# Kernel tuning notes

Measured on AMD Instinct MI355X. Metric: run time of the kernel, lower is better.

The kernel has to match this reference:

```python
import jax, jax.numpy as jnp
import numpy as np

B, S, T, E, H, Vt, Vs, M = 16, 64, 64, 256, 512, 32000, 32000, 100
J = 2 * M + 1


def _lstm(x, lengths, Wx, Wh, b, reverse=False):
    # TF LSTMCell (forget_bias=1.0) with sequence_length masking, optional reverse_sequence.
    Bn, Tn, _ = x.shape
    Hn = Wh.shape[0]
    tpos = jnp.arange(Tn)
    ridx = None
    if reverse:
        ridx = jnp.where(tpos[None, :] < lengths[:, None], lengths[:, None] - 1 - tpos[None, :], tpos[None, :])
        x = jnp.take_along_axis(x, ridx[:, :, None], axis=1)
    mask = (tpos[:, None] < lengths[None, :])[:, :, None]  # [T,B,1]
    xT = jnp.swapaxes(x, 0, 1)  # [T,B,E]

    def step(carry, inp):
        h, c = carry
        xt, mt = inp
        g = xt @ Wx + h @ Wh + b
        i, j, f, o = jnp.split(g, 4, axis=-1)
        c_new = jax.nn.sigmoid(f + 1.0) * c + jax.nn.sigmoid(i) * jnp.tanh(j)
        h_new = jax.nn.sigmoid(o) * jnp.tanh(c_new)
        c2 = jnp.where(mt, c_new, c)
        h2 = jnp.where(mt, h_new, h)
        return (h2, c2), jnp.where(mt, h_new, jnp.zeros_like(h_new))

    init = (jnp.zeros((Bn, Hn), x.dtype), jnp.zeros((Bn, Hn), x.dtype))
    _, ys = jax.lax.scan(step, init, (xT, mask))
    ys = jnp.swapaxes(ys, 0, 1)  # [B,T,H]
    if reverse:
        ys = jnp.take_along_axis(ys, ridx[:, :, None], axis=1)
    return ys


def setup_inputs() -> dict:
    key = jax.random.key(0)
    ks = jax.random.split(key, 24)
    sc = 0.05
    n = lambda k, shape: (jax.random.normal(k, shape, jnp.float32) * sc)
    inp = {
        "sources": jax.random.randint(ks[0], (B, S), 0, Vs, jnp.int32),
        "targets": jax.random.randint(ks[1], (B, T), 0, Vt, jnp.int32),
        "targets_null": jnp.array([Vt - 1], jnp.int32),
        "target_lengths": jax.random.randint(ks[2], (B,), T // 2, T + 1, jnp.int32),
        "emb": n(ks[3], (Vt, E)),
        "nnW": n(ks[4], (E, H)),
        "nnb": jnp.zeros((H,), jnp.float32),
        "Wx_fw": n(ks[5], (E, 4 * H)),
        "Wh_fw": n(ks[6], (H, 4 * H)),
        "b_fw": jnp.zeros((4 * H,), jnp.float32),
        "Wx_bw": n(ks[7], (E, 4 * H)),
        "Wh_bw": n(ks[8], (H, 4 * H)),
        "b_bw": jnp.zeros((4 * H,), jnp.float32),
        "Wproj_e": n(ks[9], (2 * H, H)),
        "Wv": n(ks[10], (H, Vs)),
        "bv": jnp.zeros((Vs,), jnp.float32),
        "Wproj_t": n(ks[11], (2 * H, E)),
        "Wj": n(ks[12], (H, J)),
        "bj": jnp.zeros((J,), jnp.float32),
        "Wp0": n(ks[13], (H, 1)),
        "bp0": jnp.zeros((1,), jnp.float32),
    }
    return inp


def reference(sources, targets, targets_null, target_lengths, emb, nnW, nnb,
              Wx_fw, Wh_fw, b_fw, Wx_bw, Wh_bw, b_bw, Wproj_e, Wv, bv,
              Wproj_t, Wj, bj, Wp0, bp0):
    x = emb[targets]                              # [B,T,E]
    x_null = emb[targets_null]                    # [1,E]
    null_state = jnp.tanh(x_null @ nnW + nnb)     # [1,H]
    h_fw = _lstm(x, target_lengths, Wx_fw, Wh_fw, b_fw, False)
    h_bw = _lstm(x, target_lengths, Wx_bw, Wh_bw, b_bw, True)
    h_cat = jnp.concatenate([h_fw, h_bw], axis=-1)  # [B,T,2H]

    # ---- emission ----
    ts = h_cat @ Wproj_e                          # [B,T,H]
    probs = jax.nn.softmax(ts @ Wv + bv, axis=-1)             # [B,T,Vs]
    null_probs = jax.nn.softmax(null_state @ Wv + bv, axis=-1)  # [1,Vs]
    e_word = jnp.take_along_axis(probs, sources[:, None, :].astype(jnp.int32), axis=2)  # [B,T,S]
    e_null = jnp.broadcast_to(null_probs[0][sources][:, None, :], e_word.shape)
    emission = jnp.concatenate([e_word, e_null], axis=1)       # [B,2T,S]

    # ---- transition ----
    tt = jnp.tanh((h_cat @ Wproj_t) @ nnW + nnb)  # [B,T,H]
    jump = jax.nn.softmax(tt @ Wj + bj, axis=-1)  # [B,T,J]
    p0 = jax.nn.sigmoid(tt @ Wp0 + bp0)[..., 0]   # [B,T]
    Tn = targets.shape[1]
    # entry (i,j) <- jump[i, M + j - i] (the tf.map_fn gather over word_idx)
    idx = M + jnp.arange(Tn)[None, :] - jnp.arange(Tn)[:, None]  # [T,T]
    jw = jnp.take_along_axis(jump, jnp.broadcast_to(idx[None], (jump.shape[0], Tn, Tn)), axis=2)  # [B,T,T]
    eye = jnp.eye(Tn, dtype=jw.dtype)
    half = jnp.concatenate([jw, p0[:, :, None] * eye], axis=2)            # [B,T,2T]
    transition = jnp.concatenate([half, half], axis=1)                    # [B,2T,2T]
    lhalf = jnp.concatenate([jnp.log(jw), jnp.log(p0)[:, :, None] * eye], axis=2)
    transition_log = jnp.concatenate([lhalf, lhalf], axis=1)
    return emission, transition, transition_log
```

## Files before the change

kernel.cpp:

```cpp
#include <hip/hip_runtime.h>
#include <hip/hip_bf16.h>
#include <math.h>

#define Bn 16
#define Sn 64
#define Tn 64
#define En 256
#define Hn 512
#define VS 32000
#define Jn 201
#define Mn 100

#define O_HCATF  0
#define O_DENOM  524288
#define O_NULLD  525312
#define O_SLOTS  525376
#define O_HBUF   527424
#define ZERO_N   560192
#define O_NS     560192
#define O_TS     560704
#define O_TSF    1084992
#define O_TTPRE  1347136
#define O_TTPF   1609280
#define O_TT     1740352
#define O_XF     2264640
#define O_WVC    2264640
#define O_WXFW   2395712
#define O_WXBW   2657856
#define O_WPEF   2920000
#define O_WPTF   3182144
#define O_NNWF   3313216
#define O_GX     3378752

typedef __attribute__((ext_vector_type(8))) short short8;
typedef __attribute__((ext_vector_type(4))) float f32x4;

__device__ __forceinline__ float sigf(float x) { return 1.0f / (1.0f + expf(-x)); }
__device__ __forceinline__ unsigned short tobf(float x) {
    __hip_bfloat16 h = __float2bfloat16(x);
    return *reinterpret_cast<unsigned short*>(&h);
}

__device__ __forceinline__ void dconvA(const float* __restrict__ A, uint4* __restrict__ out,
                                       int K, const int* __restrict__ gidx, int g) {
    int Kd = K >> 5;
    int lane = g & 63, t = g >> 6;
    int ks = t % Kd, mt = t / Kd;
    int m = mt * 16 + (lane & 15);
    int k0 = ks * 32 + (lane >> 4) * 8;
    const float* p = (gidx ? A + (size_t)gidx[m] * K : A + (size_t)m * K) + k0;
    float4 f0 = *(const float4*)(p);
    float4 f1 = *(const float4*)(p + 4);
    unsigned short u[8] = {tobf(f0.x), tobf(f0.y), tobf(f0.z), tobf(f0.w),
                           tobf(f1.x), tobf(f1.y), tobf(f1.z), tobf(f1.w)};
    out[g] = *(uint4*)u;
}

__device__ __forceinline__ void dconvB(const float* __restrict__ B, uint4* __restrict__ out,
                                       int N, int K, int g) {
    int Kd = K >> 5;
    int lane = g & 63, t = g >> 6;
    int ks = t % Kd, nt = t / Kd;
    int n = nt * 16 + (lane & 15);
    int k0 = ks * 32 + (lane >> 4) * 8;
    const float* p = B + (size_t)k0 * N + n;
    unsigned short u[8];
#pragma unroll
    for (int j = 0; j < 8; j++) u[j] = tobf(p[(size_t)j * N]);
    out[g] = *(uint4*)u;
}

__global__ __launch_bounds__(256) void convA2_k(const float* __restrict__ ttpre,
                                                uint4* __restrict__ ttpf,
                                                const float* __restrict__ ts,
                                                uint4* __restrict__ tsf) {
    int blk = blockIdx.x, tid = threadIdx.x;
    if (blk < 128) dconvA(ttpre, ttpf, 256, nullptr, blk * 256 + tid);
    else           dconvA(ts, tsf, 512, nullptr, (blk - 128) * 256 + tid);
}

__global__ __launch_bounds__(256) void mega_prep_k(float4* __restrict__ zdst, int zn4,
                                                   const float* __restrict__ emb,
                                                   const int* __restrict__ targets,
                                                   uint4* __restrict__ xf,
                                                   const float* __restrict__ wxfw, uint4* __restrict__ wxfwf,
                                                   const float* __restrict__ wxbw, uint4* __restrict__ wxbwf) {
    int blk = blockIdx.x, tid = threadIdx.x;
    if (blk < 548) {
        int i = blk * 256 + tid;
        if (i < zn4) zdst[i] = make_float4(0.f, 0.f, 0.f, 0.f);
    } else if (blk < 676) {
        dconvA(emb, xf, 256, targets, (blk - 548) * 256 + tid);
    } else if (blk < 932) {
        dconvB(wxfw, wxfwf, 2048, 256, (blk - 676) * 256 + tid);
    } else {
        dconvB(wxbw, wxbwf, 2048, 256, (blk - 932) * 256 + tid);
    }
}

template <int ACT>
__device__ __forceinline__ void gemm_body(const uint4* __restrict__ af,
                                          const uint4* __restrict__ bf,
                                          const float* __restrict__ bias,
                                          float* __restrict__ C, int N, int Kd,
                                          int bx, int by) {
    int tid = threadIdx.x, w = tid >> 6, lane = tid & 63;
    int ntb = bx * 8 + w * 2;
    int mtb = by * 8;
    f32x4 acc[8][2];
#pragma unroll
    for (int i = 0; i < 8; i++)
#pragma unroll
        for (int j = 0; j < 2; j++) acc[i][j] = 0.0f;
    for (int ks = 0; ks < Kd; ++ks) {
        uint4 b0 = bf[(size_t)(ntb * Kd + ks) * 64 + lane];
        uint4 b1 = bf[(size_t)((ntb + 1) * Kd + ks) * 64 + lane];
#pragma unroll
        for (int i = 0; i < 8; i++) {
            uint4 a = af[(size_t)((mtb + i) * Kd + ks) * 64 + lane];
            acc[i][0] = __builtin_amdgcn_mfma_f32_16x16x32_bf16(
                *reinterpret_cast<short8*>(&a), *reinterpret_cast<short8*>(&b0), acc[i][0], 0, 0, 0);
            acc[i][1] = __builtin_amdgcn_mfma_f32_16x16x32_bf16(
                *reinterpret_cast<short8*>(&a), *reinterpret_cast<short8*>(&b1), acc[i][1], 0, 0, 0);
        }
    }
    int n0 = ntb * 16 + (lane & 15);
    int q = lane >> 4;
    float bs0 = bias ? bias[n0] : 0.f;
    float bs1 = bias ? bias[n0 + 16] : 0.f;
#pragma unroll
    for (int i = 0; i < 8; i++)
#pragma unroll
        for (int r = 0; r < 4; r++) {
            int m = (mtb + i) * 16 + q * 4 + r;
            float v0 = acc[i][0][r] + bs0;
            float v1 = acc[i][1][r] + bs1;
            if (ACT == 1) { v0 = tanhf(v0); v1 = tanhf(v1); }
            C[(size_t)m * N + n0] = v0;
            C[(size_t)m * N + n0 + 16] = v1;
        }
}

template <int ACT>
__global__ __launch_bounds__(256) void gemm_mfma_k(const uint4* __restrict__ af,
                                                   const uint4* __restrict__ bf,
                                                   const float* __restrict__ bias,
                                                   float* __restrict__ C, int N, int Kd) {
    gemm_body<ACT>(af, bf, bias, C, N, Kd, blockIdx.x, blockIdx.y);
}

__global__ __launch_bounds__(256) void gx_gemm_k(const uint4* __restrict__ xf,
                                                 const uint4* __restrict__ wxfwf,
                                                 const uint4* __restrict__ wxbwf,
                                                 const float* __restrict__ b_fw,
                                                 const float* __restrict__ b_bw,
                                                 float* __restrict__ gx) {
    int bx = blockIdx.x;
    if (bx < 16) gemm_body<0>(xf, wxfwf, b_fw, gx, 2048, 8, bx, blockIdx.y);
    else         gemm_body<0>(xf, wxbwf, b_bw, gx + 2097152, 2048, 8, bx - 16, blockIdx.y);
}

__global__ __launch_bounds__(256) void proj_gemm_k(const uint4* __restrict__ hcatf,
                                                   const uint4* __restrict__ wpef,
                                                   const uint4* __restrict__ wptf,
                                                   float* __restrict__ ts,
                                                   float* __restrict__ ttpre) {
    int bx = blockIdx.x;
    if (bx < 4) gemm_body<0>(hcatf, wpef, nullptr, ts, 512, 32, bx, blockIdx.y);
    else        gemm_body<0>(hcatf, wptf, nullptr, ttpre, 256, 32, bx - 4, blockIdx.y);
}

__global__ __launch_bounds__(256, 1) void lstm_fused_k(const float* __restrict__ wh_fw,
                                                       const float* __restrict__ wh_bw,
                                                       const float* __restrict__ gx,
                                                       const int* __restrict__ lengths,
                                                       unsigned* __restrict__ hbuf32,
                                                       unsigned* __restrict__ hcat32,
                                                       unsigned* __restrict__ slots,
                                                       const float* __restrict__ Wv,
                                                       const float* __restrict__ emb,
                                                       const int* __restrict__ tnull,
                                                       const float* __restrict__ nnW,
                                                       const float* __restrict__ nnb,
                                                       const float* __restrict__ bv,
                                                       float* __restrict__ ns,
                                                       float* __restrict__ nd,
                                                       const int* __restrict__ sources,
                                                       float* __restrict__ wvc,
                                                       const float* __restrict__ wpe, uint4* __restrict__ wpef,
                                                       const float* __restrict__ wpt, uint4* __restrict__ wptf,
                                                       const float* __restrict__ nnw2, uint4* __restrict__ nnwf) {
    int blk = blockIdx.x;
    int tid = threadIdx.x;

    if (blk >= 669) {
        dconvB(nnw2, nnwf, 512, 256, (blk - 669) * 256 + tid);
        return;
    }
    if (blk >= 541) {
        dconvB(wpt, wptf, 256, 1024, (blk - 541) * 256 + tid);
        return;
    }
    if (blk >= 285) {
        dconvB(wpe, wpef, 512, 1024, (blk - 285) * 256 + tid);
        return;
    }
    if (blk >= 157) {
        int cb = blk - 157;
#pragma unroll
        for (int cc = 0; cc < 8; ++cc) {
            int ci = cb * 8 + cc;
            int c = sources[ci];
            float v0 = Wv[(size_t)tid * VS + c];
            float v1 = Wv[(size_t)(tid + 256) * VS + c];
            wvc[(size_t)ci * 512 + tid] = v0;
            wvc[(size_t)ci * 512 + 256 + tid] = v1;
        }
        return;
    }
    if (blk >= 32) {
        __shared__ float xn[En];
        __shared__ float nsl[Hn];
        __shared__ float red[4];
        int bid = blk - 32;
        xn[tid] = emb[(size_t)tnull[0] * En + tid];
        __syncthreads();
#pragma unroll
        for (int hh = 0; hh < 2; hh++) {
            int h = tid + hh * 256;
            float a = nnb[h];
            for (int e = 0; e < En; e++) a += xn[e] * nnW[(size_t)e * Hn + h];
            float v = tanhf(a);
            nsl[h] = v;
            if (bid == 0) ns[h] = v;
        }
        __syncthreads();
        int v = bid * 256 + tid;
        float a = bv[v];
        for (int k = 0; k < Hn; k++) a += nsl[k] * Wv[(size_t)k * VS + v];
        float e = expf(a);
        for (int o = 1; o < 64; o <<= 1) e += __shfl_xor(e, o);
        if ((tid & 63) == 0) red[tid >> 6] = e;
        __syncthreads();
        if (tid == 0) atomicAdd(nd, red[0] + red[1] + red[2] + red[3]);
        return;
    }

    __shared__ uint4 whf[8192];
    __shared__ float raw[32][129];
    __shared__ int lenS[16];
    int dir = blk >> 4;
    int u0 = (blk & 15) * 32;
    const float* wh = dir ? wh_bw : wh_fw;
    if (tid < 16) lenS[tid] = lengths[tid];

    for (int chunk = 0; chunk < 16; ++chunk) {
#pragma unroll
        for (int it = 0; it < 16; ++it) {
            int li = it * 256 + tid;
            int kl = li >> 7, c = li & 127;
            int g = c >> 5, ub = c & 31;
            raw[kl][c] = wh[(size_t)(chunk * 32 + kl) * 2048 + g * 512 + u0 + ub];
        }
        __syncthreads();
#pragma unroll
        for (int it = 0; it < 2; ++it) {
            int idx = tid * 2 + it;
            int w = idx >> 7, t = (idx >> 6) & 1, lane = idx & 63;
            int n = lane & 15, uu = n >> 1, p = n & 1;
            int cc = (t * 2 + p) * 32 + w * 8 + uu;
            int kb = (lane >> 4) * 8;
            unsigned short u8[8];
#pragma unroll
            for (int j = 0; j < 8; j++) u8[j] = tobf(raw[kb + j][cc]);
            whf[((w * 2 + t) * 16 + chunk) * 64 + lane] = *(uint4*)u8;
        }
        __syncthreads();
    }

    int wv = tid >> 6, lane = tid & 63;
    int n = lane & 15, uu = n >> 1, q = lane >> 4;
    int u = u0 + wv * 8 + uu;
    float creg[4] = {0.f, 0.f, 0.f, 0.f};
    unsigned short hbf[4] = {0, 0, 0, 0};

    for (int s = 0; s < 64; ++s) {
        float gxi[4], gxj[4], gxf[4], gxo[4];
#pragma unroll
        for (int r = 0; r < 4; r++) {
            int b = q * 4 + r;
            int len = lenS[b];
            int tc = dir ? (len - 1 - s) : s;
            tc = tc < 0 ? 0 : tc;
            const float* gp = gx + (size_t)dir * 2097152 + (size_t)(b * 64 + tc) * 2048 + u;
            gxi[r] = gp[0]; gxj[r] = gp[512]; gxf[r] = gp[1024]; gxo[r] = gp[1536];
        }
        const unsigned long long* hb64 =
            (const unsigned long long*)(hbuf32 + (((s & 1) * 2 + dir) * 16) * 256);
        unsigned long long h64[32];
#pragma unroll
        for (int ks = 0; ks < 16; ks++) {
            int idx = n * 128 + ks * 8 + q * 2;
            h64[2 * ks] = __hip_atomic_load(hb64 + idx, __ATOMIC_RELAXED, __HIP_MEMORY_SCOPE_AGENT);
            h64[2 * ks + 1] = __hip_atomic_load(hb64 + idx + 1, __ATOMIC_RELAXED, __HIP_MEMORY_SCOPE_AGENT);
        }
        f32x4 acc0 = {0.f, 0.f, 0.f, 0.f}, acc1 = {0.f, 0.f, 0.f, 0.f};
#pragma unroll
        for (int ks = 0; ks < 16; ks++) {
            unsigned long long av[2] = {h64[2 * ks], h64[2 * ks + 1]};
            short8 a = *reinterpret_cast<short8*>(av);
            uint4 b0 = whf[((wv * 2 + 0) * 16 + ks) * 64 + lane];
            uint4 b1 = whf[((wv * 2 + 1) * 16 + ks) * 64 + lane];
            acc0 = __builtin_amdgcn_mfma_f32_16x16x32_bf16(a, *reinterpret_cast<short8*>(&b0), acc0, 0, 0, 0);
            acc1 = __builtin_amdgcn_mfma_f32_16x16x32_bf16(a, *reinterpret_cast<short8*>(&b1), acc1, 0, 0, 0);
        }
#pragma unroll
        for (int r = 0; r < 4; r++) {
            float jvv = __shfl_xor(acc0[r], 1);
            float ovv = __shfl_xor(acc1[r], 1);
            int b = q * 4 + r;
            int len = lenS[b];
            float gi = acc0[r] + gxi[r];
            float gj = jvv + gxj[r];
            float gf = acc1[r] + gxf[r];
            float go = ovv + gxo[r];
            float cn = sigf(gf + 1.0f) * creg[r] + sigf(gi) * tanhf(gj);
            float hn = sigf(go) * tanhf(cn);
            if (s < len) { creg[r] = cn; hbf[r] = tobf(hn); }
        }
#pragma unroll
        for (int r = 0; r < 4; r++) {
            unsigned self = hbf[r];
            unsigned part = (unsigned)__shfl_xor((int)self, 2) & 0xffffu;
            if ((n & 3) == 0) {
                unsigned pk = self | (part << 16);
                int b = q * 4 + r;
                __hip_atomic_store(
                    hbuf32 + ((((s + 1) & 1) * 2 + dir) * 16 + b) * 256 + (u >> 1), pk,
                    __ATOMIC_RELAXED, __HIP_MEMORY_SCOPE_AGENT);
                int len = lenS[b];
                if (s < len) {
                    int tin = dir ? (len - 1 - s) : s;
                    int row = b * 64 + tin, col = dir * 512 + u;
                    int mt = row >> 4, ksx = col >> 5;
                    int lanep = (row & 15) | (((col >> 3) & 3) << 4);
                    hcat32[(size_t)(((mt * 32 + ksx) * 64 + lanep) * 4) + ((col & 7) >> 1)] = pk;
                }
            }
        }
        if (s == 63) break;
        __syncthreads();
        if (tid == 0)
            __hip_atomic_store(&slots[blk * 64], (unsigned)(s + 1), __ATOMIC_RELAXED,
                               __HIP_MEMORY_SCOPE_AGENT);
        if (tid < 16) {
            while (__hip_atomic_load(&slots[(dir * 16 + tid) * 64], __ATOMIC_RELAXED,
                                     __HIP_MEMORY_SCOPE_AGENT) < (unsigned)(s + 1)) {
                __builtin_amdgcn_s_sleep(1);
            }
        }
        __syncthreads();
    }
}

__global__ __launch_bounds__(256) void phaseA_mfma_k(const uint4* __restrict__ tsb,
                                                     const float* __restrict__ Wv,
                                                     const float* __restrict__ bv,
                                                     float* __restrict__ denom) {
    __shared__ uint4 wls[8192];
    __shared__ float redL[4][128];
    int tid = threadIdx.x;
    int wave = tid >> 6, lane = tid & 63;
    for (int it = 0; it < 32; ++it) {
        int g = it * 256 + tid;
        int gl = g & 63, t = g >> 6;
        int ks = t & 15, tl = t >> 4;
        int nt = blockIdx.x * 8 + tl;
        int nn = nt * 16 + (gl & 15);
        int k0 = ks * 32 + (gl >> 4) * 8;
        const float* p = Wv + (size_t)k0 * VS + nn;
        unsigned short u[8];
#pragma unroll
        for (int j = 0; j < 8; j++) u[j] = tobf(p[(size_t)j * VS]);
        wls[g] = *(uint4*)u;
    }
    __syncthreads();

    int ntbase = blockIdx.x * 8 + wave * 2;
    float bv0 = bv[ntbase * 16 + (lane & 15)];
    float bv1 = bv[(ntbase + 1) * 16 + (lane & 15)];
    int q = lane >> 4;
    for (int mc = 0; mc < 8; ++mc) {
        f32x4 acc[8][2];
#pragma unroll
        for (int i = 0; i < 8; i++)
#pragma unroll
            for (int j = 0; j < 2; j++) acc[i][j] = 0.0f;
#pragma unroll 4
        for (int ks = 0; ks < 16; ++ks) {
            short8 a[8], b[2];
#pragma unroll
            for (int i = 0; i < 8; i++) {
                int mt = mc * 8 + i;
                uint4 t = tsb[(size_t)(mt * 16 + ks) * 64 + lane];
                a[i] = *reinterpret_cast<short8*>(&t);
            }
#pragma unroll
            for (int j = 0; j < 2; j++) {
                uint4 t = wls[((wave * 2 + j) * 16 + ks) * 64 + lane];
                b[j] = *reinterpret_cast<short8*>(&t);
            }
#pragma unroll
            for (int i = 0; i < 8; i++)
#pragma unroll
                for (int j = 0; j < 2; j++)
                    acc[i][j] = __builtin_amdgcn_mfma_f32_16x16x32_bf16(a[i], b[j], acc[i][j], 0, 0, 0);
        }
#pragma unroll
        for (int i = 0; i < 8; i++) {
#pragma unroll
            for (int r = 0; r < 4; r++) {
                float e = __expf(acc[i][0][r] + bv0) + __expf(acc[i][1][r] + bv1);
                e += __shfl_xor(e, 1);
                e += __shfl_xor(e, 2);
                e += __shfl_xor(e, 4);
                e += __shfl_xor(e, 8);
                if ((lane & 15) == 0) redL[wave][i * 16 + q * 4 + r] = e;
            }
        }
        __syncthreads();
        if (tid < 128) {
            float v = redL[0][tid] + redL[1][tid] + redL[2][tid] + redL[3][tid];
            atomicAdd(&denom[mc * 128 + tid], v);
        }
        __syncthreads();
    }
}

__global__ __launch_bounds__(512) void emission_k(const float* __restrict__ ts,
                                                  const float* __restrict__ wvc,
                                                  const float* __restrict__ bv,
                                                  const int* __restrict__ sources,
                                                  const float* __restrict__ ns,
                                                  const float* __restrict__ denom,
                                                  const float* __restrict__ nulld,
                                                  float* __restrict__ em) {
    __shared__ float colv[512];
    __shared__ float red[64][9];
    __shared__ float red2[8];
    __shared__ float env_s, bvc_s;
    int b = blockIdx.y, sc = blockIdx.x;
    int tid = threadIdx.x;
    for (int qq = 0; qq < 8; ++qq) {
        int s = sc * 8 + qq;
        int ci = b * 64 + s;
        __syncthreads();
        colv[tid] = wvc[(size_t)ci * 512 + tid];
        if (tid == 0) bvc_s = bv[sources[ci]];
        __syncthreads();
        int r = tid & 63, ksl = tid >> 6;
        const float* tr = ts + (size_t)(b * 64 + r) * 512 + ksl * 64;
        float p = 0.f;
#pragma unroll
        for (int k4 = 0; k4 < 16; k4++) {
            float4 t4 = *(const float4*)(tr + k4 * 4);
            float4 c4 = *(const float4*)&colv[ksl * 64 + k4 * 4];
            p += t4.x * c4.x + t4.y * c4.y + t4.z * c4.z + t4.w * c4.w;
        }
        red[r][ksl] = p;
        if (tid < 8) {
            float pn = 0.f;
#pragma unroll
            for (int k4 = 0; k4 < 16; k4++) {
                float4 n4 = *(const float4*)(ns + tid * 64 + k4 * 4);
                float4 c4 = *(const float4*)&colv[tid * 64 + k4 * 4];
                pn += n4.x * c4.x + n4.y * c4.y + n4.z * c4.z + n4.w * c4.w;
            }
            red2[tid] = pn;
        }
        __syncthreads();
        if (tid < 64) {
            float dot = red[tid][0] + red[tid][1] + red[tid][2] + red[tid][3] +
                        red[tid][4] + red[tid][5] + red[tid][6] + red[tid][7];
            float ew = expf(dot + bvc_s) / denom[b * 64 + tid];
            em[(size_t)(b * 128 + tid) * 64 + s] = ew;
        } else if (tid == 64) {
            float dn = red2[0] + red2[1] + red2[2] + red2[3] +
                       red2[4] + red2[5] + red2[6] + red2[7];
            env_s = expf(dn + bvc_s) / nulld[0];
        }
        __syncthreads();
        if (tid < 64) em[(size_t)(b * 128 + 64 + tid) * 64 + s] = env_s;
    }
}

__global__ __launch_bounds__(256) void transition_k(const float* __restrict__ tt,
                                                    const float* __restrict__ Wj,
                                                    const float* __restrict__ bj,
                                                    const float* __restrict__ Wp0,
                                                    const float* __restrict__ bp0,
                                                    float* __restrict__ trans,
                                                    float* __restrict__ tlog) {
    __shared__ float ttl[512];
    __shared__ float jrow[Jn], ljrow[Jn];
    __shared__ float sred[256];
    __shared__ float p0_s, lp0_s;
    int blk = blockIdx.x;
    int b = blk >> 6, i = blk & 63;
    int tid = threadIdx.x;
    {
        const float* trr = tt + (size_t)blk * 512;
        if (tid < 128) *(float4*)&ttl[tid * 4] = *(const float4*)(trr + tid * 4);
    }
    __syncthreads();
    bool isj = tid < Jn;
    bool isp = tid == Jn;
    float l = 0.f;
    if (isj || isp) {
        const float* wb = isj ? (Wj + tid) : Wp0;
        int stride = isj ? Jn : 1;
        float a = isj ? bj[tid] : bp0[0];
        for (int k = 0; k < 512; k++) a += ttl[k] * wb[(size_t)k * stride];
        l = a;
    }
    sred[tid] = isj ? l : -1e30f;
    __syncthreads();
    for (int o = 128; o > 0; o >>= 1) {
        if (tid < o) sred[tid] = fmaxf(sred[tid], sred[tid + o]);
        __syncthreads();
    }
    float m = sred[0];
    __syncthreads();
    float ex = isj ? expf(l - m) : 0.f;
    sred[tid] = ex;
    __syncthreads();
    for (int o = 128; o > 0; o >>= 1) {
        if (tid < o) sred[tid] += sred[tid + o];
        __syncthreads();
    }
    float S = sred[0];
    if (isj) {
        jrow[tid] = ex / S;
        ljrow[tid] = (l - m) - logf(S);
    }
    if (isp) {
        float pv = 1.f / (1.f + expf(-l));
        p0_s = pv;
        lp0_s = logf(pv);
    }
    __syncthreads();
    if (tid < 128) {
        int j = tid;
        float tv, lv;
        if (j < 64) {
            int id = Mn + j - i;
            tv = jrow[id];
            lv = ljrow[id];
        } else {
            bool dg = (j - 64) == i;
            tv = dg ? p0_s : 0.f;
            lv = dg ? lp0_s : 0.f;
        }
        size_t r1 = (size_t)(b * 128 + i) * 128 + j;
        size_t r2 = (size_t)(b * 128 + 64 + i) * 128 + j;
        trans[r1] = tv;
        trans[r2] = tv;
        tlog[r1] = lv;
        tlog[r2] = lv;
    }
}

extern "C" void kernel_launch(void* const* d_in, const int* in_sizes, int n_in,
                              void* d_out, int out_size, void* d_ws, size_t ws_size,
                              hipStream_t stream) {
    const int* sources = (const int*)d_in[0];
    const int* targets = (const int*)d_in[1];
    const int* tnull = (const int*)d_in[2];
    const int* lengths = (const int*)d_in[3];
    const float* emb = (const float*)d_in[4];
    const float* nnW = (const float*)d_in[5];
    const float* nnb = (const float*)d_in[6];
    const float* Wx_fw = (const float*)d_in[7];
    const float* Wh_fw = (const float*)d_in[8];
    const float* b_fw = (const float*)d_in[9];
    const float* Wx_bw = (const float*)d_in[10];
    const float* Wh_bw = (const float*)d_in[11];
    const float* b_bw = (const float*)d_in[12];
    const float* Wproj_e = (const float*)d_in[13];
    const float* Wv = (const float*)d_in[14];
    const float* bv = (const float*)d_in[15];
    const float* Wproj_t = (const float*)d_in[16];
    const float* Wj = (const float*)d_in[17];
    const float* bj = (const float*)d_in[18];
    const float* Wp0 = (const float*)d_in[19];
    const float* bp0 = (const float*)d_in[20];

    float* ws = (float*)d_ws;
    float* out = (float*)d_out;
    float* out_em = out;
    float* out_tr = out + 131072;
    float* out_tl = out + 131072 + 262144;

    mega_prep_k<<<1188, 256, 0, stream>>>((float4*)ws, ZERO_N / 4,
                                          emb, targets, (uint4*)(ws + O_XF),
                                          Wx_fw, (uint4*)(ws + O_WXFW),
                                          Wx_bw, (uint4*)(ws + O_WXBW));

    gx_gemm_k<<<dim3(32, 8), 256, 0, stream>>>((uint4*)(ws + O_XF), (uint4*)(ws + O_WXFW),
                                               (uint4*)(ws + O_WXBW), b_fw, b_bw, ws + O_GX);

    lstm_fused_k<<<733, 256, 0, stream>>>(Wh_fw, Wh_bw, ws + O_GX, lengths,
                                          (unsigned*)(ws + O_HBUF), (unsigned*)(ws + O_HCATF),
                                          (unsigned*)(ws + O_SLOTS),
                                          Wv, emb, tnull, nnW, nnb, bv,
                                          ws + O_NS, ws + O_NULLD,
                                          sources, ws + O_WVC,
                                          Wproj_e, (uint4*)(ws + O_WPEF),
                                          Wproj_t, (uint4*)(ws + O_WPTF),
                                          nnW, (uint4*)(ws + O_NNWF));

    proj_gemm_k<<<dim3(6, 8), 256, 0, stream>>>((uint4*)(ws + O_HCATF), (uint4*)(ws + O_WPEF),
                                                (uint4*)(ws + O_WPTF), ws + O_TS, ws + O_TTPRE);

    convA2_k<<<384, 256, 0, stream>>>(ws + O_TTPRE, (uint4*)(ws + O_TTPF),
                                      ws + O_TS, (uint4*)(ws + O_TSF));
    gemm_mfma_k<1><<<dim3(4, 8), 256, 0, stream>>>((uint4*)(ws + O_TTPF), (uint4*)(ws + O_NNWF),
                                                   nnb, ws + O_TT, 512, 8);

    phaseA_mfma_k<<<250, 256, 0, stream>>>((const uint4*)(ws + O_TSF),
                                           Wv, bv, ws + O_DENOM);

    emission_k<<<dim3(8, 16), 512, 0, stream>>>(ws + O_TS, ws + O_WVC, bv, sources, ws + O_NS,
                                                ws + O_DENOM, ws + O_NULLD, out_em);

    transition_k<<<1024, 256, 0, stream>>>(ws + O_TT, Wj, bj, Wp0, bp0, out_tr, out_tl);
}
```

Before: 872.3 us.

## Fold Wproj_t·nnW into one weight, fuse projection, conversion and output kernels

Precomputes the combined weight Wproj_t@nnW alongside the input-gate GEMM. This removes a whole GEMM stage and its intermediate bf16 conversion, so tt is produced directly from h_cat in one MFMA pass. The projection kernel now also writes the bf16 fragment layout of ts from shared memory, replacing the separate conversion kernel. The emission and transition kernels are merged into one launch to cut launch count. The trade-off is that rounding the combined weight to bf16 changes numerics slightly, and transition blocks now run with 512 threads where only 256 do useful work.

```diff
diff --git a/kernel.cpp b/kernel.cpp
--- a/kernel.cpp
+++ b/kernel.cpp
@@ -19,16 +19,16 @@
 #define ZERO_N   560192
 #define O_NS     560192
 #define O_TS     560704
+#define O_WCOMB  560704
 #define O_TSF    1084992
-#define O_TTPRE  1347136
-#define O_TTPF   1609280
+#define O_WCOMBF 1347136
+#define O_WPTAF  1609280
 #define O_TT     1740352
 #define O_XF     2264640
 #define O_WVC    2264640
 #define O_WXFW   2395712
 #define O_WXBW   2657856
 #define O_WPEF   2920000
-#define O_WPTF   3182144
 #define O_NNWF   3313216
 #define O_GX     3378752
 
@@ -70,21 +70,14 @@
     out[g] = *(uint4*)u;
 }
 
-__global__ __launch_bounds__(256) void convA2_k(const float* __restrict__ ttpre,
-                                                uint4* __restrict__ ttpf,
-                                                const float* __restrict__ ts,
-                                                uint4* __restrict__ tsf) {
-    int blk = blockIdx.x, tid = threadIdx.x;
-    if (blk < 128) dconvA(ttpre, ttpf, 256, nullptr, blk * 256 + tid);
-    else           dconvA(ts, tsf, 512, nullptr, (blk - 128) * 256 + tid);
-}
-
 __global__ __launch_bounds__(256) void mega_prep_k(float4* __restrict__ zdst, int zn4,
                                                    const float* __restrict__ emb,
                                                    const int* __restrict__ targets,
                                                    uint4* __restrict__ xf,
                                                    const float* __restrict__ wxfw, uint4* __restrict__ wxfwf,
-                                                   const float* __restrict__ wxbw, uint4* __restrict__ wxbwf) {
+                                                   const float* __restrict__ wxbw, uint4* __restrict__ wxbwf,
+                                                   const float* __restrict__ wpt, uint4* __restrict__ wptaf,
+                                                   const float* __restrict__ nnw, uint4* __restrict__ nnwf) {
     int blk = blockIdx.x, tid = threadIdx.x;
     if (blk < 548) {
         int i = blk * 256 + tid;
@@ -93,8 +86,12 @@
         dconvA(emb, xf, 256, targets, (blk - 548) * 256 + tid);
     } else if (blk < 932) {
         dconvB(wxfw, wxfwf, 2048, 256, (blk - 676) * 256 + tid);
+    } else if (blk < 1188) {
+        dconvB(wxbw, wxbwf, 2048, 256, (blk - 932) * 256 + tid);
+    } else if (blk < 1316) {
+        dconvA(wpt, wptaf, 256, nullptr, (blk - 1188) * 256 + tid);
     } else {
-        dconvB(wxbw, wxbwf, 2048, 256, (blk - 932) * 256 + tid);
+        dconvB(nnw, nnwf, 512, 256, (blk - 1316) * 256 + tid);
     }
 }
 
@@ -141,33 +138,19 @@
         }
 }
 
-template <int ACT>
-__global__ __launch_bounds__(256) void gemm_mfma_k(const uint4* __restrict__ af,
-                                                   const uint4* __restrict__ bf,
-                                                   const float* __restrict__ bias,
-                                                   float* __restrict__ C, int N, int Kd) {
-    gemm_body<ACT>(af, bf, bias, C, N, Kd, blockIdx.x, blockIdx.y);
-}
-
-__global__ __launch_bounds__(256) void gx_gemm_k(const uint4* __restrict__ xf,
-                                                 const uint4* __restrict__ wxfwf,
-                                                 const uint4* __restrict__ wxbwf,
-                                                 const float* __restrict__ b_fw,
-                                                 const float* __restrict__ b_bw,
-                                                 float* __restrict__ gx) {
+__global__ __launch_bounds__(256) void gxw_gemm_k(const uint4* __restrict__ xf,
+                                                  const uint4* __restrict__ wxfwf,
+                                                  const uint4* __restrict__ wxbwf,
+                                                  const float* __restrict__ b_fw,
+                                                  const float* __restrict__ b_bw,
+                                                  float* __restrict__ gx,
+                                                  const uint4* __restrict__ wptaf,
+                                                  const uint4* __restrict__ nnwf,
+                                                  float* __restrict__ wcomb) {
     int bx = blockIdx.x;
-    if (bx < 16) gemm_body<0>(xf, wxfwf, b_fw, gx, 2048, 8, bx, blockIdx.y);
-    else         gemm_body<0>(xf, wxbwf, b_bw, gx + 2097152, 2048, 8, bx - 16, blockIdx.y);
-}
-
-__global__ __launch_bounds__(256) void proj_gemm_k(const uint4* __restrict__ hcatf,
-                                                   const uint4* __restrict__ wpef,
-                                                   const uint4* __restrict__ wptf,
-                                                   float* __restrict__ ts,
-                                                   float* __restrict__ ttpre) {
-    int bx = blockIdx.x;
-    if (bx < 4) gemm_body<0>(hcatf, wpef, nullptr, ts, 512, 32, bx, blockIdx.y);
-    else        gemm_body<0>(hcatf, wptf, nullptr, ttpre, 256, 32, bx - 4, blockIdx.y);
+    if (bx < 16)      gemm_body<0>(xf, wxfwf, b_fw, gx, 2048, 8, bx, blockIdx.y);
+    else if (bx < 32) gemm_body<0>(xf, wxbwf, b_bw, gx + 2097152, 2048, 8, bx - 16, blockIdx.y);
+    else              gemm_body<0>(wptaf, nnwf, nullptr, wcomb, 512, 8, bx - 32, blockIdx.y);
 }
 
 __global__ __launch_bounds__(256, 1) void lstm_fused_k(const float* __restrict__ wh_fw,
@@ -188,17 +171,12 @@
                                                        const int* __restrict__ sources,
                                                        float* __restrict__ wvc,
                                                        const float* __restrict__ wpe, uint4* __restrict__ wpef,
-                                                       const float* __restrict__ wpt, uint4* __restrict__ wptf,
-                                                       const float* __restrict__ nnw2, uint4* __restrict__ nnwf) {
+                                                       const float* __restrict__ wcomb, uint4* __restrict__ wcombf) {
     int blk = blockIdx.x;
     int tid = threadIdx.x;
 
-    if (blk >= 669) {
-        dconvB(nnw2, nnwf, 512, 256, (blk - 669) * 256 + tid);
-        return;
-    }
     if (blk >= 541) {
-        dconvB(wpt, wptf, 256, 1024, (blk - 541) * 256 + tid);
+        dconvB(wcomb, wcombf, 512, 1024, (blk - 541) * 256 + tid);
         return;
     }
     if (blk >= 285) {
@@ -363,6 +341,83 @@
     }
 }
 
+__global__ __launch_bounds__(256) void proj2_k(const uint4* __restrict__ hcatf,
+                                               const uint4* __restrict__ wpef,
+                                               const uint4* __restrict__ wcombf,
+                                               const float* __restrict__ nnb,
+                                               float* __restrict__ ts,
+                                               uint4* __restrict__ tsf,
+                                               float* __restrict__ tt) {
+    __shared__ float smem[128][130];
+    int bx = blockIdx.x, by = blockIdx.y;
+    int tid = threadIdx.x, w = tid >> 6, lane = tid & 63;
+    bool is_ts = bx < 4;
+    int bxl = is_ts ? bx : bx - 4;
+    const uint4* bf = is_ts ? wpef : wcombf;
+    int ntb = bxl * 8 + w * 2;
+    int mtb = by * 8;
+    const int Kd = 32;
+    f32x4 acc[8][2];
+#pragma unroll
+    for (int i = 0; i < 8; i++)
+#pragma unroll
+        for (int j = 0; j < 2; j++) acc[i][j] = 0.0f;
+    for (int ks = 0; ks < Kd; ++ks) {
+        uint4 b0 = bf[(size_t)(ntb * Kd + ks) * 64 + lane];
+        uint4 b1 = bf[(size_t)((ntb + 1) * Kd + ks) * 64 + lane];
+#pragma unroll
+        for (int i = 0; i < 8; i++) {
+            uint4 a = hcatf[(size_t)((mtb + i) * Kd + ks) * 64 + lane];
+            acc[i][0] = __builtin_amdgcn_mfma_f32_16x16x32_bf16(
+                *reinterpret_cast<short8*>(&a), *reinterpret_cast<short8*>(&b0), acc[i][0], 0, 0, 0);
+            acc[i][1] = __builtin_amdgcn_mfma_f32_16x16x32_bf16(
+                *reinterpret_cast<short8*>(&a), *reinterpret_cast<short8*>(&b1), acc[i][1], 0, 0, 0);
+        }
+    }
+    int n0 = ntb * 16 + (lane & 15);
+    int q = lane >> 4;
+    if (is_ts) {
+#pragma unroll
+        for (int i = 0; i < 8; i++)
+#pragma unroll
+            for (int r = 0; r < 4; r++) {
+                int m = (mtb + i) * 16 + q * 4 + r;
+                int lm = i * 16 + q * 4 + r;
+                int lc = (w * 2) * 16 + (lane & 15);
+                float v0 = acc[i][0][r];
+                float v1 = acc[i][1][r];
+                ts[(size_t)m * 512 + n0] = v0;
+                ts[(size_t)m * 512 + n0 + 16] = v1;
+                smem[lm][lc] = v0;
+                smem[lm][lc + 16] = v1;
+            }
+        __syncthreads();
+#pragma unroll
+        for (int e = 0; e < 8; ++e) {
+            int fi = tid * 8 + e;
+            int lf = fi & 63, t2 = fi >> 6;
+            int ksl = t2 & 3, mtl = t2 >> 2;
+            int row = mtl * 16 + (lf & 15);
+            int col = ksl * 32 + (lf >> 4) * 8;
+            unsigned short u8[8];
+#pragma unroll
+            for (int j = 0; j < 8; j++) u8[j] = tobf(smem[row][col + j]);
+            tsf[((size_t)(by * 8 + mtl) * 16 + (bx * 4 + ksl)) * 64 + lf] = *(uint4*)u8;
+        }
+    } else {
+        float bs0 = nnb[n0];
+        float bs1 = nnb[n0 + 16];
+#pragma unroll
+        for (int i = 0; i < 8; i++)
+#pragma unroll
+            for (int r = 0; r < 4; r++) {
+                int m = (mtb + i) * 16 + q * 4 + r;
+                tt[(size_t)m * 512 + n0] = tanhf(acc[i][0][r] + bs0);
+                tt[(size_t)m * 512 + n0 + 16] = tanhf(acc[i][1][r] + bs1);
+            }
+    }
+}
+
 __global__ __launch_bounds__(256) void phaseA_mfma_k(const uint4* __restrict__ tsb,
                                                      const float* __restrict__ Wv,
                                                      const float* __restrict__ bv,
@@ -437,79 +492,80 @@
     }
 }
 
-__global__ __launch_bounds__(512) void emission_k(const float* __restrict__ ts,
-                                                  const float* __restrict__ wvc,
-                                                  const float* __restrict__ bv,
-                                                  const int* __restrict__ sources,
-                                                  const float* __restrict__ ns,
-                                                  const float* __restrict__ denom,
-                                                  const float* __restrict__ nulld,
-                                                  float* __restrict__ em) {
-    __shared__ float colv[512];
-    __shared__ float red[64][9];
-    __shared__ float red2[8];
-    __shared__ float env_s, bvc_s;
-    int b = blockIdx.y, sc = blockIdx.x;
+__global__ __launch_bounds__(512) void emtr_k(const float* __restrict__ ts,
+                                              const float* __restrict__ wvc,
+                                              const float* __restrict__ bv,
+                                              const int* __restrict__ sources,
+                                              const float* __restrict__ ns,
+                                              const float* __restrict__ denom,
+                                              const float* __restrict__ nulld,
+                                              float* __restrict__ em,
+                                              const float* __restrict__ tt,
+                                              const float* __restrict__ Wj,
+                                              const float* __restrict__ bj,
+                                              const float* __restrict__ Wp0,
+                                              const float* __restrict__ bp0,
+                                              float* __restrict__ trans,
+                                              float* __restrict__ tlog) {
+    int blk = blockIdx.x;
     int tid = threadIdx.x;
-    for (int qq = 0; qq < 8; ++qq) {
-        int s = sc * 8 + qq;
-        int ci = b * 64 + s;
-        __syncthreads();
-        colv[tid] = wvc[(size_t)ci * 512 + tid];
-        if (tid == 0) bvc_s = bv[sources[ci]];
-        __syncthreads();
-        int r = tid & 63, ksl = tid >> 6;
-        const float* tr = ts + (size_t)(b * 64 + r) * 512 + ksl * 64;
-        float p = 0.f;
-#pragma unroll
-        for (int k4 = 0; k4 < 16; k4++) {
-            float4 t4 = *(const float4*)(tr + k4 * 4);
-            float4 c4 = *(const float4*)&colv[ksl * 64 + k4 * 4];
-            p += t4.x * c4.x + t4.y * c4.y + t4.z * c4.z + t4.w * c4.w;
-        }
-        red[r][ksl] = p;
-        if (tid < 8) {
-            float pn = 0.f;
+    if (blk < 128) {
+        __shared__ float colv[512];
+        __shared__ float red[64][9];
+        __shared__ float red2[8];
+        __shared__ float env_s, bvc_s;
+        int b = blk >> 3, sc = blk & 7;
+        for (int qq = 0; qq < 8; ++qq) {
+            int s = sc * 8 + qq;
+            int ci = b * 64 + s;
+            __syncthreads();
+            colv[tid] = wvc[(size_t)ci * 512 + tid];
+            if (tid == 0) bvc_s = bv[sources[ci]];
+            __syncthreads();
+            int r = tid & 63, ksl = tid >> 6;
+            const float* tr = ts + (size_t)(b * 64 + r) * 512 + ksl * 64;
+            float p = 0.f;
 #pragma unroll
             for (int k4 = 0; k4 < 16; k4++) {
-                float4 n4 = *(const float4*)(ns + tid * 64 + k4 * 4);
-                float4 c4 = *(const float4*)&colv[tid * 64 + k4 * 4];
-                pn += n4.x * c4.x + n4.y * c4.y + n4.z * c4.z + n4.w * c4.w;
-            }
-            red2[tid] = pn;
-        }
-        __syncthreads();
-        if (tid < 64) {
-            float dot = red[tid][0] + red[tid][1] + red[tid][2] + red[tid][3] +
-                        red[tid][4] + red[tid][5] + red[tid][6] + red[tid][7];
-            float ew = expf(dot + bvc_s) / denom[b * 64 + tid];
-            em[(size_t)(b * 128 + tid) * 64 + s] = ew;
-        } else if (tid == 64) {
-            float dn = red2[0] + red2[1] + red2[2] + red2[3] +
-                       red2[4] + red2[5] + red2[6] + red2[7];
-            env_s = expf(dn + bvc_s) / nulld[0];
-        }
-        __syncthreads();
-        if (tid < 64) em[(size_t)(b * 128 + 64 + tid) * 64 + s] = env_s;
-    }
-}
-
-__global__ __launch_bounds__(256) void transition_k(const float* __restrict__ tt,
-                                                    const float* __restrict__ Wj,
-                                                    const float* __restrict__ bj,
-                                                    const float* __restrict__ Wp0,
-                                                    const float* __restrict__ bp0,
-                                                    float* __restrict__ trans,
-                                                    float* __restrict__ tlog) {
+                float4 t4 = *(const float4*)(tr + k4 * 4);
+                float4 c4 = *(const float4*)&colv[ksl * 64 + k4 * 4];
+                p += t4.x * c4.x + t4.y * c4.y + t4.z * c4.z + t4.w * c4.w;
+            }
+            red[r][ksl] = p;
+            if (tid < 8) {
+                float pn = 0.f;
+#pragma unroll
+                for (int k4 = 0; k4 < 16; k4++) {
+                    float4 n4 = *(const float4*)(ns + tid * 64 + k4 * 4);
+                    float4 c4 = *(const float4*)&colv[tid * 64 + k4 * 4];
+                    pn += n4.x * c4.x + n4.y * c4.y + n4.z * c4.z + n4.w * c4.w;
+                }
+                red2[tid] = pn;
+            }
+            __syncthreads();
+            if (tid < 64) {
+                float dot = red[tid][0] + red[tid][1] + red[tid][2] + red[tid][3] +
+                            red[tid][4] + red[tid][5] + red[tid][6] + red[tid][7];
+                float ew = expf(dot + bvc_s) / denom[b * 64 + tid];
+                em[(size_t)(b * 128 + tid) * 64 + s] = ew;
+            } else if (tid == 64) {
+                float dn = red2[0] + red2[1] + red2[2] + red2[3] +
+                           red2[4] + red2[5] + red2[6] + red2[7];
+                env_s = expf(dn + bvc_s) / nulld[0];
+            }
+            __syncthreads();
+            if (tid < 64) em[(size_t)(b * 128 + 64 + tid) * 64 + s] = env_s;
+        }
+        return;
+    }
     __shared__ float ttl[512];
     __shared__ float jrow[Jn], ljrow[Jn];
     __shared__ float sred[256];
     __shared__ float p0_s, lp0_s;
-    int blk = blockIdx.x;
-    int b = blk >> 6, i = blk & 63;
-    int tid = threadIdx.x;
+    int tb = blk - 128;
+    int b = tb >> 6, i = tb & 63;
     {
-        const float* trr = tt + (size_t)blk * 512;
+        const float* trr = tt + (size_t)tb * 512;
         if (tid < 128) *(float4*)&ttl[tid * 4] = *(const float4*)(trr + tid * 4);
     }
     __syncthreads();
@@ -523,7 +579,7 @@
         for (int k = 0; k < 512; k++) a += ttl[k] * wb[(size_t)k * stride];
         l = a;
     }
-    sred[tid] = isj ? l : -1e30f;
+    if (tid < 256) sred[tid] = isj ? l : -1e30f;
     __syncthreads();
     for (int o = 128; o > 0; o >>= 1) {
         if (tid < o) sred[tid] = fmaxf(sred[tid], sred[tid + o]);
@@ -532,7 +588,7 @@
     float m = sred[0];
     __syncthreads();
     float ex = isj ? expf(l - m) : 0.f;
-    sred[tid] = ex;
+    if (tid < 256) sred[tid] = ex;
     __syncthreads();
     for (int o = 128; o > 0; o >>= 1) {
         if (tid < o) sred[tid] += sred[tid + o];
@@ -601,37 +657,34 @@
     float* out_tr = out + 131072;
     float* out_tl = out + 131072 + 262144;
 
-    mega_prep_k<<<1188, 256, 0, stream>>>((float4*)ws, ZERO_N / 4,
+    mega_prep_k<<<1380, 256, 0, stream>>>((float4*)ws, ZERO_N / 4,
                                           emb, targets, (uint4*)(ws + O_XF),
                                           Wx_fw, (uint4*)(ws + O_WXFW),
-                                          Wx_bw, (uint4*)(ws + O_WXBW));
-
-    gx_gemm_k<<<dim3(32, 8), 256, 0, stream>>>((uint4*)(ws + O_XF), (uint4*)(ws + O_WXFW),
-                                               (uint4*)(ws + O_WXBW), b_fw, b_bw, ws + O_GX);
-
-    lstm_fused_k<<<733, 256, 0, stream>>>(Wh_fw, Wh_bw, ws + O_GX, lengths,
+                                          Wx_bw, (uint4*)(ws + O_WXBW),
+                                          Wproj_t, (uint4*)(ws + O_WPTAF),
+                                          nnW, (uint4*)(ws + O_NNWF));
+
+    gxw_gemm_k<<<dim3(36, 8), 256, 0, stream>>>((uint4*)(ws + O_XF), (uint4*)(ws + O_WXFW),
+                                                (uint4*)(ws + O_WXBW), b_fw, b_bw, ws + O_GX,
+                                                (uint4*)(ws + O_WPTAF), (uint4*)(ws + O_NNWF),
+                                                ws + O_WCOMB);
+
+    lstm_fused_k<<<797, 256, 0, stream>>>(Wh_fw, Wh_bw, ws + O_GX, lengths,
                                           (unsigned*)(ws + O_HBUF), (unsigned*)(ws + O_HCATF),
                                           (unsigned*)(ws + O_SLOTS),
                                           Wv, emb, tnull, nnW, nnb, bv,
                                           ws + O_NS, ws + O_NULLD,
                                           sources, ws + O_WVC,
                                           Wproj_e, (uint4*)(ws + O_WPEF),
-                                          Wproj_t, (uint4*)(ws + O_WPTF),
-                                          nnW, (uint4*)(ws + O_NNWF));
-
-    proj_gemm_k<<<dim3(6, 8), 256, 0, stream>>>((uint4*)(ws + O_HCATF), (uint4*)(ws + O_WPEF),
-                                                (uint4*)(ws + O_WPTF), ws + O_TS, ws + O_TTPRE);
-
-    convA2_k<<<384, 256, 0, stream>>>(ws + O_TTPRE, (uint4*)(ws + O_TTPF),
-                                      ws + O_TS, (uint4*)(ws + O_TSF));
-    gemm_mfma_k<1><<<dim3(4, 8), 256, 0, stream>>>((uint4*)(ws + O_TTPF), (uint4*)(ws + O_NNWF),
-                                                   nnb, ws + O_TT, 512, 8);
-
-    phaseA_mfma_k<<<250, 256, 0, stream>>>((const uint4*)(ws + O_TSF),
-                                           Wv, bv, ws + O_DENOM);
-
-    emission_k<<<dim3(8, 16), 512, 0, stream>>>(ws + O_TS, ws + O_WVC, bv, sources, ws + O_NS,
-                                                ws + O_DENOM, ws + O_NULLD, out_em);
-
-    transition_k<<<1024, 256, 0, stream>>>(ws + O_TT, Wj, bj, Wp0, bp0, out_tr, out_tl);
-}
+                                          ws + O_WCOMB, (uint4*)(ws + O_WCOMBF));
+
+    proj2_k<<<dim3(8, 8), 256, 0, stream>>>((uint4*)(ws + O_HCATF), (uint4*)(ws + O_WPEF),
+                                            (uint4*)(ws + O_WCOMBF), nnb,
+                                            ws + O_TS, (uint4*)(ws + O_TSF), ws + O_TT);
+
+    phaseA_mfma_k<<<250, 256, 0, stream>>>((const uint4*)(ws + O_TSF), Wv, bv, ws + O_DENOM);
+
+    emtr_k<<<1152, 512, 0, stream>>>(ws + O_TS, ws + O_WVC, bv, sources, ws + O_NS,
+                                     ws + O_DENOM, ws + O_NULLD, out_em,
+                                     ws + O_TT, Wj, bj, Wp0, bp0, out_tr, out_tl);
+}
```

After: 897.5 us. 2.9% more time.
